# Performance work log

Measured on AMD Instinct MI355X. Metric: run time of the kernel, lower is better.

The kernel has to match this reference:

```python
import jax, jax.numpy as jnp
import numpy as np

N_NODES = 50000
N_EDGES = 1_600_000
IN_FEATS = 256
N_HEADS = 2
OUT_FEATS = 64
NEG_SLOPE = 0.2


def setup_inputs() -> dict:
    key = jax.random.key(0)
    k1, k2, k3, k4, k5, k6 = jax.random.split(key, 6)
    feat = jax.random.normal(k1, (N_NODES, IN_FEATS), dtype=jnp.float32)
    src = jax.random.randint(k2, (N_EDGES,), 0, N_NODES, dtype=jnp.int32)
    dst = jax.random.randint(k3, (N_EDGES,), 0, N_NODES, dtype=jnp.int32)
    W = jax.random.normal(k4, (IN_FEATS, N_HEADS * OUT_FEATS), dtype=jnp.float32) * 0.05
    attn_l = jax.random.normal(k5, (N_HEADS, OUT_FEATS), dtype=jnp.float32) * 0.1
    attn_r = jax.random.normal(k6, (N_HEADS, OUT_FEATS), dtype=jnp.float32) * 0.1
    return {"feat": feat, "src": src, "dst": dst, "W": W, "attn_l": attn_l, "attn_r": attn_r}


def reference(feat, src, dst, W, attn_l, attn_r):
    # node projection: [N, H, F]
    ft = (feat @ W).reshape(N_NODES, N_HEADS, OUT_FEATS)
    el = jnp.einsum('nhf,hf->nh', ft, attn_l)  # [N, H]
    er = jnp.einsum('nhf,hf->nh', ft, attn_r)  # [N, H]
    # per-edge logits + leaky relu
    e = el[src] + er[dst]                      # [E, H]
    e = jnp.where(e > 0, e, NEG_SLOPE * e)
    # segment softmax over incoming edges of each dst node
    m = jax.ops.segment_max(e, dst, num_segments=N_NODES)     # [N, H]
    m = jnp.where(jnp.isfinite(m), m, 0.0)                     # guard empty segments
    e_exp = jnp.exp(e - jax.lax.stop_gradient(m)[dst])         # [E, H]
    s = jax.ops.segment_sum(e_exp, dst, num_segments=N_NODES)  # [N, H]
    a = e_exp / jnp.maximum(s[dst], 1e-20)                     # [E, H]
    # scatter-weighted aggregation: sum_e a_e * ft[src_e] into dst
    msg = ft[src] * a[:, :, None]                              # [E, H, F]
    rst = jax.ops.segment_sum(msg, dst, num_segments=N_NODES)  # [N, H, F]
    return rst
```

## Files before the change

### kernel.cpp

```cpp
#include <hip/hip_runtime.h>
#include <hip/hip_fp16.h>

#define N_NODES 50000
#define N_EDGES 1600000
#define IN_F 256
#define NEG_SLOPE 0.2f
#define CHUNK 1024
#define NCH ((N_NODES + CHUNK - 1) / CHUNK)
#define NPAD 50048
#define NCOPY 8

typedef _Float16 f16x8 __attribute__((ext_vector_type(8)));
typedef float f32x4 __attribute__((ext_vector_type(4)));

__global__ __launch_bounds__(256) void k_gemm(const float* __restrict__ feat,
                                              const float* __restrict__ W,
                                              const float* __restrict__ attn_l,
                                              const float* __restrict__ attn_r,
                                              __half* __restrict__ ft16,
                                              float* __restrict__ el,
                                              float* __restrict__ er) {
  __shared__ __align__(16) _Float16 Wt[4 * 128 * 8];
  __shared__ __align__(16) _Float16 Fl[64 * 40];
  const int tid = threadIdx.x;
  const int lane = tid & 63;
  const int w = tid >> 6;
  const int c0 = lane & 15;
  const int g = lane >> 4;
  const int row0 = blockIdx.x * 64;

  f32x4 acc[8];
#pragma unroll
  for (int t = 0; t < 8; ++t) acc[t] = f32x4{0.f, 0.f, 0.f, 0.f};

  const int fr = tid >> 2;
  const int fk = (tid & 3) * 8;
  const int wc = tid & 127;
  const int wgp = tid >> 7;

  for (int kt = 0; kt < IN_F; kt += 32) {
    __syncthreads();
    {
      int grow = row0 + fr;
      if (grow >= N_NODES) grow = N_NODES - 1;
      const float* fp = feat + (size_t)grow * IN_F + kt + fk;
      float4 v0 = *(const float4*)fp;
      float4 v1 = *(const float4*)(fp + 4);
      f16x8 h;
      h[0] = (_Float16)v0.x; h[1] = (_Float16)v0.y;
      h[2] = (_Float16)v0.z; h[3] = (_Float16)v0.w;
      h[4] = (_Float16)v1.x; h[5] = (_Float16)v1.y;
      h[6] = (_Float16)v1.z; h[7] = (_Float16)v1.w;
      *(f16x8*)&Fl[fr * 40 + fk] = h;
    }
#pragma unroll
    for (int gg = 0; gg < 2; ++gg) {
      int gw = wgp * 2 + gg;
      f16x8 h;
#pragma unroll
      for (int j = 0; j < 8; ++j)
        h[j] = (_Float16)W[(size_t)(kt + gw * 8 + j) * 128 + wc];
      *(f16x8*)&Wt[(gw * 128 + wc) * 8] = h;
    }
    __syncthreads();
    f16x8 a = *(const f16x8*)&Fl[(w * 16 + c0) * 40 + g * 8];
#pragma unroll
    for (int t = 0; t < 8; ++t) {
      f16x8 b = *(const f16x8*)&Wt[(g * 128 + t * 16 + c0) * 8];
      acc[t] = __builtin_amdgcn_mfma_f32_16x16x32_f16(a, b, acc[t], 0, 0, 0);
    }
  }

  float al8[8], ar8[8];
#pragma unroll
  for (int t = 0; t < 8; ++t) {
    al8[t] = attn_l[t * 16 + c0];
    ar8[t] = attn_r[t * 16 + c0];
  }
#pragma unroll
  for (int r = 0; r < 4; ++r) {
    int row = row0 + w * 16 + g * 4 + r;
    float sl0 = 0.f, sl1 = 0.f, sr0 = 0.f, sr1 = 0.f;
#pragma unroll
    for (int t = 0; t < 4; ++t) {
      sl0 = fmaf(acc[t][r], al8[t], sl0);
      sr0 = fmaf(acc[t][r], ar8[t], sr0);
    }
#pragma unroll
    for (int t = 4; t < 8; ++t) {
      sl1 = fmaf(acc[t][r], al8[t], sl1);
      sr1 = fmaf(acc[t][r], ar8[t], sr1);
    }
#pragma unroll
    for (int m = 1; m < 16; m <<= 1) {
      sl0 += __shfl_xor(sl0, m, 64);
      sl1 += __shfl_xor(sl1, m, 64);
      sr0 += __shfl_xor(sr0, m, 64);
      sr1 += __shfl_xor(sr1, m, 64);
    }
    if (row < N_NODES) {
#pragma unroll
      for (int t = 0; t < 8; ++t)
        ft16[(size_t)row * 128 + t * 16 + c0] = __float2half(acc[t][r]);
      if (c0 == 0) {
        el[row * 2 + 0] = sl0; el[row * 2 + 1] = sl1;
        er[row * 2 + 0] = sr0; er[row * 2 + 1] = sr1;
      }
    }
  }
}

__global__ __launch_bounds__(256) void k_deg(const int* __restrict__ dst,
                                             int* __restrict__ deg8,
                                             ushort* __restrict__ rank) {
  int t = blockIdx.x * 256 + threadIdx.x;
  if (t >= N_EDGES / 4) return;
  int* mydeg = deg8 + (blockIdx.x & 7) * NPAD;
  int4 d4 = ((const int4*)dst)[t];
  ushort4 r;
  r.x = (ushort)atomicAdd(&mydeg[d4.x], 1);
  r.y = (ushort)atomicAdd(&mydeg[d4.y], 1);
  r.z = (ushort)atomicAdd(&mydeg[d4.z], 1);
  r.w = (ushort)atomicAdd(&mydeg[d4.w], 1);
  ((ushort4*)rank)[t] = r;
}

__global__ __launch_bounds__(256) void k_scanA(const int* __restrict__ deg8,
                                               int* __restrict__ csum) {
  __shared__ int ws[4];
  int b = blockIdx.x, tid = threadIdx.x, lane = tid & 63, w = tid >> 6;
  int i0 = b * CHUNK + tid * 4;
  int s = 0;
#pragma unroll
  for (int c = 0; c < NCOPY; ++c) {
    const int* dp = deg8 + c * NPAD;
#pragma unroll
    for (int j = 0; j < 4; ++j) {
      int i = i0 + j;
      if (i < N_NODES) s += dp[i];
    }
  }
#pragma unroll
  for (int m = 32; m > 0; m >>= 1) s += __shfl_xor(s, m, 64);
  if (lane == 0) ws[w] = s;
  __syncthreads();
  if (tid == 0) csum[b] = ws[0] + ws[1] + ws[2] + ws[3];
}

__global__ void k_scanB(const int* __restrict__ csum, int* __restrict__ coff,
                        int* __restrict__ rowptr) {
  int tid = threadIdx.x;
  int v = (tid < NCH) ? csum[tid] : 0;
  int x = v;
#pragma unroll
  for (int off = 1; off < 64; off <<= 1) {
    int y = __shfl_up(x, off, 64);
    if (tid >= off) x += y;
  }
  if (tid < NCH) coff[tid] = x - v;
  if (tid == NCH - 1) rowptr[N_NODES] = x;
}

__global__ __launch_bounds__(256) void k_scanC(const int* __restrict__ deg8,
                                               const int* __restrict__ coff,
                                               int* __restrict__ rowptr) {
  __shared__ int wtot[4];
  int b = blockIdx.x, tid = threadIdx.x, lane = tid & 63, w = tid >> 6;
  int i0 = b * CHUNK + tid * 4;
  int d[4] = {0, 0, 0, 0};
#pragma unroll
  for (int c = 0; c < NCOPY; ++c) {
    const int* dp = deg8 + c * NPAD;
#pragma unroll
    for (int j = 0; j < 4; ++j)
      if (i0 + j < N_NODES) d[j] += dp[i0 + j];
  }
  int t1 = d[0] + d[1], t2 = t1 + d[2], t3 = t2 + d[3];
  int x = t3;
#pragma unroll
  for (int off = 1; off < 64; off <<= 1) {
    int y = __shfl_up(x, off, 64);
    if (lane >= off) x += y;
  }
  if (lane == 63) wtot[w] = x;
  __syncthreads();
  int woff = 0;
  for (int j = 0; j < w; ++j) woff += wtot[j];
  int excl = coff[b] + woff + (x - t3);
  int pre[4] = {0, d[0], t1, t2};
#pragma unroll
  for (int j = 0; j < 4; ++j) {
    int i = i0 + j;
    if (i < N_NODES) rowptr[i] = excl + pre[j];
  }
}

__global__ __launch_bounds__(256) void k_off8(const int* __restrict__ deg8,
                                              const int* __restrict__ rowptr,
                                              int* __restrict__ off8) {
  int d = blockIdx.x * 256 + threadIdx.x;
  if (d >= N_NODES) return;
  int run = rowptr[d];
#pragma unroll
  for (int c = 0; c < NCOPY; ++c) {
    off8[c * NPAD + d] = run;
    run += deg8[c * NPAD + d];
  }
}

__device__ __forceinline__ void sort1(int s, int d, int rk,
                                      const int* __restrict__ myoff,
                                      const float2* __restrict__ el2,
                                      const float2* __restrict__ er2,
                                      unsigned long long* __restrict__ rec) {
  float2 a = el2[s];
  float2 b = er2[d];
  float e0 = a.x + b.x, e1 = a.y + b.y;
  e0 = e0 > 0.f ? e0 : NEG_SLOPE * e0;
  e1 = e1 > 0.f ? e1 : NEG_SLOPE * e1;
  __half2 h = __floats2half2_rn(__expf(e0), __expf(e1));
  unsigned long long v =
      ((unsigned long long)(*(unsigned*)&h) << 32) | (unsigned)s;
  rec[myoff[d] + rk] = v;
}

__global__ __launch_bounds__(256) void k_sortp(const int* __restrict__ src,
                                               const int* __restrict__ dst,
                                               const ushort* __restrict__ rank,
                                               const int* __restrict__ off8,
                                               const float2* __restrict__ el2,
                                               const float2* __restrict__ er2,
                                               unsigned long long* __restrict__ rec) {
  int t = blockIdx.x * 256 + threadIdx.x;
  if (t >= N_EDGES / 4) return;
  const int* myoff = off8 + (blockIdx.x & 7) * NPAD;
  int4 s4 = ((const int4*)src)[t];
  int4 d4 = ((const int4*)dst)[t];
  ushort4 r4 = ((const ushort4*)rank)[t];
  sort1(s4.x, d4.x, r4.x, myoff, el2, er2, rec);
  sort1(s4.y, d4.y, r4.y, myoff, el2, er2, rec);
  sort1(s4.z, d4.z, r4.z, myoff, el2, er2, rec);
  sort1(s4.w, d4.w, r4.w, myoff, el2, er2, rec);
}

__global__ __launch_bounds__(256) void k_agg(const unsigned long long* __restrict__ rec,
                                             const int* __restrict__ rowptr,
                                             const __half2* __restrict__ ft2,
                                             float2* __restrict__ out) {
  int t = blockIdx.x * 256 + threadIdx.x;
  int node = t >> 6, lane = t & 63;
  if (node >= N_NODES) return;
  int beg = rowptr[node], end = rowptr[node + 1];
  bool h1 = lane >= 32;
  float ax = 0.f, ay = 0.f, s = 0.f;
  int i = beg;
  for (; i + 8 <= end; i += 8) {
    unsigned long long r[8];
#pragma unroll
    for (int j = 0; j < 8; ++j) r[j] = __builtin_nontemporal_load(&rec[i + j]);
    __half2 f[8];
#pragma unroll
    for (int j = 0; j < 8; ++j)
      f[j] = ft2[(size_t)(unsigned)(r[j] & 0xffffffffu) * 64 + lane];
#pragma unroll
    for (int j = 0; j < 8; ++j) {
      unsigned pw = (unsigned)(r[j] >> 32);
      float2 p = __half22float2(*(const __half2*)&pw);
      float a = h1 ? p.y : p.x;
      float2 g = __half22float2(f[j]);
      ax = fmaf(a, g.x, ax); ay = fmaf(a, g.y, ay);
      s += a;
    }
  }
  for (; i < end; ++i) {
    unsigned long long r = rec[i];
    unsigned pw = (unsigned)(r >> 32);
    float2 p = __half22float2(*(const __half2*)&pw);
    float a = h1 ? p.y : p.x;
    float2 g = __half22float2(ft2[(size_t)(unsigned)(r & 0xffffffffu) * 64 + lane]);
    ax = fmaf(a, g.x, ax); ay = fmaf(a, g.y, ay);
    s += a;
  }
  float inv = 1.f / fmaxf(s, 1e-20f);
  out[(size_t)node * 64 + lane] = make_float2(ax * inv, ay * inv);
}

extern "C" void kernel_launch(void* const* d_in, const int* in_sizes, int n_in,
                              void* d_out, int out_size, void* d_ws, size_t ws_size,
                              hipStream_t stream) {
  const float* feat   = (const float*)d_in[0];
  const int*   src    = (const int*)d_in[1];
  const int*   dst    = (const int*)d_in[2];
  const float* W      = (const float*)d_in[3];
  const float* attn_l = (const float*)d_in[4];
  const float* attn_r = (const float*)d_in[5];
  float* out = (float*)d_out;

  char* base = (char*)d_ws;
  size_t off = 0;
  auto bump = [&](size_t bytes) -> void* {
    void* p = base + off;
    off = (off + bytes + 255) & ~(size_t)255;
    return p;
  };
  __half* ft16   = (__half*)bump(sizeof(__half) * N_NODES * 128);
  float*  el     = (float*)bump(sizeof(float) * N_NODES * 2);
  float*  er     = (float*)bump(sizeof(float) * N_NODES * 2);
  int*    deg8   = (int*)bump(sizeof(int) * NCOPY * NPAD);
  int*    off8   = (int*)bump(sizeof(int) * NCOPY * NPAD);
  int*    csum   = (int*)bump(sizeof(int) * NCH);
  int*    coff   = (int*)bump(sizeof(int) * NCH);
  int*    rowptr = (int*)bump(sizeof(int) * (N_NODES + 1));
  ushort* rank   = (ushort*)bump(sizeof(ushort) * N_EDGES);
  unsigned long long* rec =
      (unsigned long long*)bump(sizeof(unsigned long long) * N_EDGES);
  (void)ws_size; (void)in_sizes; (void)n_in; (void)out_size;

  (void)hipMemsetAsync(deg8, 0, sizeof(int) * NCOPY * NPAD, stream);

  k_deg<<<(N_EDGES / 4 + 255) / 256, 256, 0, stream>>>(dst, deg8, rank);
  k_gemm<<<(N_NODES + 63) / 64, 256, 0, stream>>>(feat, W, attn_l, attn_r, ft16, el, er);
  k_scanA<<<NCH, 256, 0, stream>>>(deg8, csum);
  k_scanB<<<1, 64, 0, stream>>>(csum, coff, rowptr);
  k_scanC<<<NCH, 256, 0, stream>>>(deg8, coff, rowptr);
  k_off8<<<(N_NODES + 255) / 256, 256, 0, stream>>>(deg8, rowptr, off8);
  k_sortp<<<(N_EDGES / 4 + 255) / 256, 256, 0, stream>>>(src, dst, rank, off8,
      (const float2*)el, (const float2*)er, rec);
  k_agg<<<(N_NODES * 64 + 255) / 256, 256, 0, stream>>>(rec, rowptr,
      (const __half2*)ft16, (float2*)out);
}
```

Measured before the change: 301.8 us.

## Replace stored edge ranks with atomic cursors in scatter; fuse off8 into scan

The degree kernel no longer writes a per-edge rank array. The scatter kernel instead claims slots with atomicAdd on per-copy cursor arrays initialised from off8, which is now produced inside k_scanC, so k_off8 is removed. Edge kernels handle 2048 edges per block and write records with nontemporal stores. This removes the rank write and read traffic and one launch, at the cost of a second round of atomics in the scatter and a nondeterministic order within each segment.

```diff
diff --git a/kernel.cpp b/kernel.cpp
--- a/kernel.cpp
+++ b/kernel.cpp
@@ -9,6 +9,8 @@
 #define NCH ((N_NODES + CHUNK - 1) / CHUNK)
 #define NPAD 50048
 #define NCOPY 8
+#define EPB 2048
+#define NEB ((N_EDGES + EPB - 1) / EPB)
 
 typedef _Float16 f16x8 __attribute__((ext_vector_type(8)));
 typedef float f32x4 __attribute__((ext_vector_type(4)));
@@ -111,18 +113,20 @@
 }
 
 __global__ __launch_bounds__(256) void k_deg(const int* __restrict__ dst,
-                                             int* __restrict__ deg8,
-                                             ushort* __restrict__ rank) {
-  int t = blockIdx.x * 256 + threadIdx.x;
-  if (t >= N_EDGES / 4) return;
+                                             int* __restrict__ deg8) {
   int* mydeg = deg8 + (blockIdx.x & 7) * NPAD;
-  int4 d4 = ((const int4*)dst)[t];
-  ushort4 r;
-  r.x = (ushort)atomicAdd(&mydeg[d4.x], 1);
-  r.y = (ushort)atomicAdd(&mydeg[d4.y], 1);
-  r.z = (ushort)atomicAdd(&mydeg[d4.z], 1);
-  r.w = (ushort)atomicAdd(&mydeg[d4.w], 1);
-  ((ushort4*)rank)[t] = r;
+  int base4 = blockIdx.x * (EPB / 4) + threadIdx.x;
+#pragma unroll
+  for (int h = 0; h < 2; ++h) {
+    int i4 = base4 + h * 256;
+    if (i4 < N_EDGES / 4) {
+      int4 d4 = ((const int4*)dst)[i4];
+      atomicAdd(&mydeg[d4.x], 1);
+      atomicAdd(&mydeg[d4.y], 1);
+      atomicAdd(&mydeg[d4.z], 1);
+      atomicAdd(&mydeg[d4.w], 1);
+    }
+  }
 }
 
 __global__ __launch_bounds__(256) void k_scanA(const int* __restrict__ deg8,
@@ -163,17 +167,22 @@
 
 __global__ __launch_bounds__(256) void k_scanC(const int* __restrict__ deg8,
                                                const int* __restrict__ coff,
-                                               int* __restrict__ rowptr) {
+                                               int* __restrict__ rowptr,
+                                               int* __restrict__ off8) {
   __shared__ int wtot[4];
   int b = blockIdx.x, tid = threadIdx.x, lane = tid & 63, w = tid >> 6;
   int i0 = b * CHUNK + tid * 4;
+  int dc[NCOPY][4];
   int d[4] = {0, 0, 0, 0};
 #pragma unroll
   for (int c = 0; c < NCOPY; ++c) {
     const int* dp = deg8 + c * NPAD;
 #pragma unroll
-    for (int j = 0; j < 4; ++j)
-      if (i0 + j < N_NODES) d[j] += dp[i0 + j];
+    for (int j = 0; j < 4; ++j) {
+      int v = (i0 + j < N_NODES) ? dp[i0 + j] : 0;
+      dc[c][j] = v;
+      d[j] += v;
+    }
   }
   int t1 = d[0] + d[1], t2 = t1 + d[2], t3 = t2 + d[3];
   int x = t3;
@@ -191,25 +200,20 @@
 #pragma unroll
   for (int j = 0; j < 4; ++j) {
     int i = i0 + j;
-    if (i < N_NODES) rowptr[i] = excl + pre[j];
-  }
-}
-
-__global__ __launch_bounds__(256) void k_off8(const int* __restrict__ deg8,
-                                              const int* __restrict__ rowptr,
-                                              int* __restrict__ off8) {
-  int d = blockIdx.x * 256 + threadIdx.x;
-  if (d >= N_NODES) return;
-  int run = rowptr[d];
-#pragma unroll
-  for (int c = 0; c < NCOPY; ++c) {
-    off8[c * NPAD + d] = run;
-    run += deg8[c * NPAD + d];
-  }
-}
-
-__device__ __forceinline__ void sort1(int s, int d, int rk,
-                                      const int* __restrict__ myoff,
+    if (i < N_NODES) {
+      int run = excl + pre[j];
+      rowptr[i] = run;
+#pragma unroll
+      for (int c = 0; c < NCOPY; ++c) {
+        off8[c * NPAD + i] = run;
+        run += dc[c][j];
+      }
+    }
+  }
+}
+
+__device__ __forceinline__ void sort1(int s, int d,
+                                      int* __restrict__ mycur,
                                       const float2* __restrict__ el2,
                                       const float2* __restrict__ er2,
                                       unsigned long long* __restrict__ rec) {
@@ -221,26 +225,30 @@
   __half2 h = __floats2half2_rn(__expf(e0), __expf(e1));
   unsigned long long v =
       ((unsigned long long)(*(unsigned*)&h) << 32) | (unsigned)s;
-  rec[myoff[d] + rk] = v;
+  int pos = atomicAdd(&mycur[d], 1);
+  __builtin_nontemporal_store(v, &rec[pos]);
 }
 
 __global__ __launch_bounds__(256) void k_sortp(const int* __restrict__ src,
                                                const int* __restrict__ dst,
-                                               const ushort* __restrict__ rank,
-                                               const int* __restrict__ off8,
+                                               int* __restrict__ off8,
                                                const float2* __restrict__ el2,
                                                const float2* __restrict__ er2,
                                                unsigned long long* __restrict__ rec) {
-  int t = blockIdx.x * 256 + threadIdx.x;
-  if (t >= N_EDGES / 4) return;
-  const int* myoff = off8 + (blockIdx.x & 7) * NPAD;
-  int4 s4 = ((const int4*)src)[t];
-  int4 d4 = ((const int4*)dst)[t];
-  ushort4 r4 = ((const ushort4*)rank)[t];
-  sort1(s4.x, d4.x, r4.x, myoff, el2, er2, rec);
-  sort1(s4.y, d4.y, r4.y, myoff, el2, er2, rec);
-  sort1(s4.z, d4.z, r4.z, myoff, el2, er2, rec);
-  sort1(s4.w, d4.w, r4.w, myoff, el2, er2, rec);
+  int* mycur = off8 + (blockIdx.x & 7) * NPAD;
+  int base4 = blockIdx.x * (EPB / 4) + threadIdx.x;
+#pragma unroll
+  for (int h = 0; h < 2; ++h) {
+    int i4 = base4 + h * 256;
+    if (i4 < N_EDGES / 4) {
+      int4 s4 = ((const int4*)src)[i4];
+      int4 d4 = ((const int4*)dst)[i4];
+      sort1(s4.x, d4.x, mycur, el2, er2, rec);
+      sort1(s4.y, d4.y, mycur, el2, er2, rec);
+      sort1(s4.z, d4.z, mycur, el2, er2, rec);
+      sort1(s4.w, d4.w, mycur, el2, er2, rec);
+    }
+  }
 }
 
 __global__ __launch_bounds__(256) void k_agg(const unsigned long long* __restrict__ rec,
@@ -311,20 +319,18 @@
   int*    csum   = (int*)bump(sizeof(int) * NCH);
   int*    coff   = (int*)bump(sizeof(int) * NCH);
   int*    rowptr = (int*)bump(sizeof(int) * (N_NODES + 1));
-  ushort* rank   = (ushort*)bump(sizeof(ushort) * N_EDGES);
   unsigned long long* rec =
       (unsigned long long*)bump(sizeof(unsigned long long) * N_EDGES);
   (void)ws_size; (void)in_sizes; (void)n_in; (void)out_size;
 
   (void)hipMemsetAsync(deg8, 0, sizeof(int) * NCOPY * NPAD, stream);
 
-  k_deg<<<(N_EDGES / 4 + 255) / 256, 256, 0, stream>>>(dst, deg8, rank);
+  k_deg<<<NEB, 256, 0, stream>>>(dst, deg8);
   k_gemm<<<(N_NODES + 63) / 64, 256, 0, stream>>>(feat, W, attn_l, attn_r, ft16, el, er);
   k_scanA<<<NCH, 256, 0, stream>>>(deg8, csum);
   k_scanB<<<1, 64, 0, stream>>>(csum, coff, rowptr);
-  k_scanC<<<NCH, 256, 0, stream>>>(deg8, coff, rowptr);
-  k_off8<<<(N_NODES + 255) / 256, 256, 0, stream>>>(deg8, rowptr, off8);
-  k_sortp<<<(N_EDGES / 4 + 255) / 256, 256, 0, stream>>>(src, dst, rank, off8,
+  k_scanC<<<NCH, 256, 0, stream>>>(deg8, coff, rowptr, off8);
+  k_sortp<<<NEB, 256, 0, stream>>>(src, dst, off8,
       (const float2*)el, (const float2*)er, rec);
   k_agg<<<(N_NODES * 64 + 255) / 256, 256, 0, stream>>>(rec, rowptr,
       (const __half2*)ft16, (float2*)out);
```

After: 354.2 us. 1.17x slower.
